# Performance work log

Hardware: AMD Instinct MI355X
Metric: run time of the kernel (lower is better)

## Reference

```python
import jax, jax.numpy as jnp
import numpy as np

VOCAB, EMBED, HIDDEN, POL = 32000, 300, 1024, 3
BS, SEQ = 64, 512


def setup_inputs() -> dict:
    key = jax.random.key(0)
    ks = jax.random.split(key, 17)
    stdv = 1.0 / np.sqrt(HIDDEN)
    u = lambda k, shape: jax.random.uniform(k, shape, jnp.float32, -stdv, stdv)
    return {
        "text": jax.random.randint(ks[0], (BS, SEQ), 0, VOCAB),
        "embed_table": jax.random.normal(ks[1], (VOCAB, EMBED), jnp.float32),
        "U_i": u(ks[2], (EMBED, HIDDEN)), "U_f": u(ks[3], (EMBED, HIDDEN)),
        "U_c": u(ks[4], (EMBED, HIDDEN)), "U_o": u(ks[5], (EMBED, HIDDEN)),
        "V_i": u(ks[6], (HIDDEN, HIDDEN)), "V_f": u(ks[7], (HIDDEN, HIDDEN)),
        "V_c": u(ks[8], (HIDDEN, HIDDEN)), "V_o": u(ks[9], (HIDDEN, HIDDEN)),
        "b_i": u(ks[10], (HIDDEN,)), "b_f": u(ks[11], (HIDDEN,)),
        "b_c": u(ks[12], (HIDDEN,)), "b_o": u(ks[13], (HIDDEN,)),
        "W_dense": u(ks[14], (HIDDEN, POL)),
        "b_dense": u(ks[15], (POL,)),
    }


def _lstm_final_h(x, U_i, U_f, U_c, U_o, V_i, V_f, V_c, V_o, b_i, b_f, b_c, b_o):
    # x: [B, S, E]. Precompute all input projections once (big fused GEMM),
    # leaving only the recurrent h @ V matmuls inside the scan.
    bs = x.shape[0]
    H = V_i.shape[0]
    U = jnp.concatenate([U_i, U_f, U_c, U_o], axis=1)          # [E, 4H]
    b = jnp.concatenate([b_i, b_f, b_c, b_o], axis=0)          # [4H]
    xU = jnp.einsum('bse,eh->sbh', x, U) + b                   # [S, B, 4H]
    V = jnp.concatenate([V_i, V_f, V_c, V_o], axis=1)          # [H, 4H]

    def step(carry, xu_t):
        h, c = carry
        gates = xu_t + h @ V                                   # [B, 4H]
        xi, xf, xg, xo = jnp.split(gates, 4, axis=-1)
        i = jax.nn.sigmoid(xi)
        f = jax.nn.sigmoid(xf)
        g = jnp.tanh(xg)
        o = jax.nn.sigmoid(xo)
        c = f * c + i * g
        h = o * jnp.tanh(c)
        return (h, c), None

    h0 = jnp.zeros((bs, H), x.dtype)
    c0 = jnp.zeros((bs, H), x.dtype)
    (h_n, c_n), _ = jax.lax.scan(step, (h0, c0), xU)
    return h_n


def reference(text, embed_table, U_i, U_f, U_c, U_o, V_i, V_f, V_c, V_o,
              b_i, b_f, b_c, b_o, W_dense, b_dense):
    x = embed_table[text]                                      # [B, S, E]
    h_n = _lstm_final_h(x, U_i, U_f, U_c, U_o, V_i, V_f, V_c, V_o,
                        b_i, b_f, b_c, b_o)                    # [B, H]
    return h_n @ W_dense + b_dense                             # [B, POL]
```

## Files before the change

kernel.cpp:

```cpp
#include <hip/hip_runtime.h>
#include <stdint.h>

#define SEQL 512
#define BATCH 64
#define EMB 300
#define EMBP 320
#define HID 1024
#define NWG 64
#define UNITS 16
#define NCH 42

typedef __attribute__((ext_vector_type(8))) short short8;
typedef __attribute__((ext_vector_type(4))) float f32x4;
typedef __attribute__((ext_vector_type(2))) unsigned int uint2v;

union Frag { short8 v; ushort u[8]; uint uu[4]; };
struct AF { uint2v lo, hi; };

__device__ __forceinline__ ushort f2bf(float f){
  union { float f; uint u; } c; c.f = f;
  return (ushort)((c.u + 0x7fffu + ((c.u >> 16) & 1u)) >> 16);
}

struct Params {
  const ushort* xbf;
  ushort* hbuf;
  float*  hfinal;
  int*    flags;
  ushort* wpack;
  const float* V[4];
  const float* U[4];
  const float* bia[4];
  const float* Wd;
  const float* bd;
  float* out;
};

__global__ void __launch_bounds__(256) prep(const int* __restrict__ text,
                                            const float* __restrict__ tab,
                                            ushort* __restrict__ xbf,
                                            ushort* __restrict__ hbuf,
                                            int* __restrict__ flags){
  const int tid = blockIdx.x * blockDim.x + threadIdx.x;
  const int nth = gridDim.x * blockDim.x;
  uint* hz = (uint*)hbuf;
  for (int i = tid; i < NWG*64*16/2; i += nth) hz[i] = 0u;
  if (tid < NWG) flags[tid] = 0;
  const int nch = SEQL*BATCH*(EMBP/8);
  for (int ch = tid; ch < nch; ch += nth){
    const int e8 = ch % (EMBP/8);
    const int sb = ch / (EMBP/8);
    const int b  = sb & (BATCH-1);
    const int s  = sb >> 6;
    const int tok = text[b*SEQL + s];
    union { ushort u[8]; uint4 v; } o;
    #pragma unroll
    for (int j = 0; j < 8; j++){
      const int e = e8*8 + j;
      o.u[j] = f2bf(e < EMB ? tab[(size_t)tok*EMB + e] : 0.f);
    }
    *(uint4*)&xbf[(size_t)sb*EMBP + e8*8] = o.v;
  }
}

__global__ void __launch_bounds__(256) packw(Params p){
  const int bid  = blockIdx.x;
  const int w    = bid / NCH;
  const int kc   = bid % NCH;
  const int tid  = threadIdx.x;
  const int nt   = tid >> 6;
  const int lane = tid & 63;
  const int l4   = (lane >> 4) & 3;
  const int colg = w*UNITS + (lane & 15);
  Frag fr;
  #pragma unroll
  for (int j = 0; j < 8; j++){
    const int koff = ((j >> 2) << 4) + l4*4 + (j & 3);
    float v = 0.f;
    if (kc < 32){
      v = p.V[nt][(size_t)(kc*32 + koff)*HID + colg];
    } else {
      const int krow = (kc-32)*32 + koff;
      if (krow < EMB) v = p.U[nt][(size_t)krow*HID + colg];
    }
    fr.u[j] = f2bf(v);
  }
  *(short8*)&p.wpack[(((size_t)(w*NCH + kc)*4 + nt)*64 + lane)*8] = fr.v;
}

#define WISSUE(c) { \
    const ushort* wp_ = wpk + (size_t)(wave + 4*(c))*2048 + lane*8; \
    asm volatile("global_load_dwordx4 %0, %4, off\n\t" \
                 "global_load_dwordx4 %1, %4, off offset:1024\n\t" \
                 "global_load_dwordx4 %2, %4, off offset:2048\n\t" \
                 "global_load_dwordx4 %3, %4, off offset:3072" \
                 : "=v"(wfr[(c)&3][0]), "=v"(wfr[(c)&3][1]), \
                   "=v"(wfr[(c)&3][2]), "=v"(wfr[(c)&3][3]) \
                 : "v"(wp_) : "memory"); }

#define VISSUE(c) { \
    const ushort* bp_ = hcur + (size_t)(wave + 4*(c))*2048 + qk; \
    _Pragma("unroll") \
    for (int m_ = 0; m_ < 4; m_++){ \
      const ushort* rp_ = bp_ + (m_*16 + mrow)*16; \
      asm volatile("global_load_dwordx2 %0, %2, off sc0 sc1\n\t" \
                   "global_load_dwordx2 %1, %2, off offset:2048 sc0 sc1" \
                   : "=v"(afr[(c)&3][m_].lo), "=v"(afr[(c)&3][m_].hi) \
                   : "v"(rp_) : "memory"); \
    } }

#define VWAIT(n) { asm volatile("s_waitcnt vmcnt(" #n ")" ::: "memory"); \
                   __builtin_amdgcn_sched_barrier(0); }

#define VMFMA(c) { \
    _Pragma("unroll") \
    for (int m_ = 0; m_ < 4; m_++){ \
      Frag a_; \
      a_.uu[0] = afr[(c)&3][m_].lo[0]; a_.uu[1] = afr[(c)&3][m_].lo[1]; \
      a_.uu[2] = afr[(c)&3][m_].hi[0]; a_.uu[3] = afr[(c)&3][m_].hi[1]; \
      _Pragma("unroll") \
      for (int nt_ = 0; nt_ < 4; nt_++) \
        acc[m_][nt_] = __builtin_amdgcn_mfma_f32_16x16x32_bf16(a_.v, wfr[(c)&3][nt_], acc[m_][nt_], 0, 0, 0); \
    } }

__global__ void __launch_bounds__(256, 1) lstm_scan(Params p){
  __shared__ float buffer[2][64][68];
  __shared__ float cst[UNITS][BATCH];
  __shared__ float bias_l[64];

  const int w    = blockIdx.x;
  const int tid  = threadIdx.x;
  const int wave = tid >> 6;
  const int lane = tid & 63;
  const int n0   = w * UNITS;
  const int mrow = lane & 15;
  const int qk   = ((lane >> 4) & 3) << 2;
  const int nU   = (wave < 2) ? 3 : 2;
  const ushort* __restrict__ wpk = p.wpack + (size_t)w*NCH*2048;

  const int pl   = lane & 15;
  const int* fp  = p.flags + 2*(wave + 4*(pl >> 1)) + (pl & 1);

  if (tid < 64) bias_l[tid] = p.bia[tid >> 4][n0 + (tid & 15)];
  for (int i = tid; i < UNITS*BATCH; i += 256) (&cst[0][0])[i] = 0.f;
  __syncthreads();

  for (int t = 0; t < SEQL; t++){
    const ushort* __restrict__ xt = p.xbf + (size_t)t * (BATCH*EMBP);

    f32x4 acc[4][4];
    #pragma unroll
    for (int m = 0; m < 4; m++)
      #pragma unroll
      for (int nt = 0; nt < 4; nt++)
        acc[m][nt] = (f32x4){0.f, 0.f, 0.f, 0.f};

    #pragma unroll
    for (int j3 = 0; j3 < 3; j3++){
      if (j3 < nU){
        const int kb  = (wave + 4*j3)*32;
        const int kcg = 32 + wave + 4*j3;
        Frag af[4];
        #pragma unroll
        for (int m = 0; m < 4; m++){
          const ushort* rp = xt + (size_t)(m*16 + mrow)*EMBP + kb + qk;
          uint2 lo = *(const uint2*)rp;
          uint2 hi = *(const uint2*)(rp + 16);
          af[m].uu[0] = lo.x; af[m].uu[1] = lo.y;
          af[m].uu[2] = hi.x; af[m].uu[3] = hi.y;
        }
        short8 wu[4];
        #pragma unroll
        for (int nt = 0; nt < 4; nt++)
          wu[nt] = *(const short8*)&wpk[(size_t)kcg*2048 + nt*512 + lane*8];
        #pragma unroll
        for (int m = 0; m < 4; m++)
          #pragma unroll
          for (int nt = 0; nt < 4; nt++)
            acc[m][nt] = __builtin_amdgcn_mfma_f32_16x16x32_bf16(af[m].v, wu[nt], acc[m][nt], 0, 0, 0);
      }
    }

    if (t > 0){
      for (;;){
        int v;
        asm volatile("global_load_dword %0, %1, off sc0 sc1\n\t"
                     "s_waitcnt vmcnt(0)"
                     : "=v"(v) : "v"(fp) : "memory");
        if (__all(v >= t)) break;
        __builtin_amdgcn_s_sleep(1);
      }
      __builtin_amdgcn_sched_barrier(0);

      const ushort* __restrict__ hcur = p.hbuf + (size_t)(t & 1) * (NWG*64*16);
      AF afr[4][4];
      short8 wfr[4][4];
      WISSUE(0) VISSUE(0) WISSUE(1) VISSUE(1)
      WISSUE(2) VISSUE(2) WISSUE(3) VISSUE(3)
      VWAIT(36) VMFMA(0) WISSUE(4) VISSUE(4)
      VWAIT(36) VMFMA(1) WISSUE(5) VISSUE(5)
      VWAIT(36) VMFMA(2) WISSUE(6) VISSUE(6)
      VWAIT(36) VMFMA(3) WISSUE(7) VISSUE(7)
      VWAIT(36) VMFMA(4)
      VWAIT(24) VMFMA(5)
      VWAIT(12) VMFMA(6)
      VWAIT(0)  VMFMA(7)
    }

    const int fq = (lane >> 4) << 2;
    if (wave >= 2){
      #pragma unroll
      for (int m = 0; m < 4; m++)
        #pragma unroll
        for (int nt = 0; nt < 4; nt++)
          *(f32x4*)&buffer[wave-2][nt*16 + mrow][m*16 + fq] = acc[m][nt];
    }
    __syncthreads();
    if (wave < 2){
      #pragma unroll
      for (int m = 0; m < 4; m++)
        #pragma unroll
        for (int nt = 0; nt < 4; nt++){
          f32x4 o = *(f32x4*)&buffer[wave][nt*16 + mrow][m*16 + fq];
          o += acc[m][nt];
          *(f32x4*)&buffer[wave][nt*16 + mrow][m*16 + fq] = o;
        }
    }
    __syncthreads();

    const int eb = tid & 63;
    const int uq = tid >> 6;
    ushort* __restrict__ hnxt = p.hbuf + (size_t)((t+1) & 1) * (NWG*64*16);
    ushort hout[4]; float hfv[4];
    #pragma unroll
    for (int rr = 0; rr < 4; rr++){
      const int u = uq*4 + rr;
      float g0 = buffer[0][ 0+u][eb] + buffer[1][ 0+u][eb] + bias_l[ 0+u];
      float g1 = buffer[0][16+u][eb] + buffer[1][16+u][eb] + bias_l[16+u];
      float g2 = buffer[0][32+u][eb] + buffer[1][32+u][eb] + bias_l[32+u];
      float g3 = buffer[0][48+u][eb] + buffer[1][48+u][eb] + bias_l[48+u];
      float ig = 1.f/(1.f + __expf(-g0));
      float fg = 1.f/(1.f + __expf(-g1));
      float gg = 2.f/(1.f + __expf(-2.f*g2)) - 1.f;
      float og = 1.f/(1.f + __expf(-g3));
      float cv = fg * cst[u][eb] + ig * gg;
      cst[u][eb] = cv;
      float hv = og * (2.f/(1.f + __expf(-2.f*cv)) - 1.f);
      hout[rr] = f2bf(hv);
      hfv[rr] = hv;
    }
    {
      union { ushort u[4]; uint2v v; } pk;
      pk.u[0]=hout[0]; pk.u[1]=hout[1]; pk.u[2]=hout[2]; pk.u[3]=hout[3];
      ushort* sa = &hnxt[(size_t)w*1024 + eb*16 + uq*4];
      asm volatile("global_store_dwordx2 %0, %1, off sc0 sc1"
                   :: "v"(sa), "v"(pk.v) : "memory");
      if (t == SEQL-1){
        f32x4 fv; fv[0]=hfv[0]; fv[1]=hfv[1]; fv[2]=hfv[2]; fv[3]=hfv[3];
        float* fa = &p.hfinal[(size_t)eb*HID + n0 + uq*4];
        asm volatile("global_store_dwordx4 %0, %1, off sc0 sc1"
                     :: "v"(fa), "v"(fv) : "memory");
      }
    }
    asm volatile("s_waitcnt vmcnt(0)" ::: "memory");
    __syncthreads();
    if (tid == 0){
      int tv = t + 1;
      asm volatile("global_store_dword %0, %1, off sc0 sc1"
                   :: "v"(p.flags + w), "v"(tv) : "memory");
    }
  }

  if (wave == 0){
    const int* ffp = p.flags + lane;
    for (;;){
      int v;
      asm volatile("global_load_dword %0, %1, off sc0 sc1\n\t"
                   "s_waitcnt vmcnt(0)"
                   : "=v"(v) : "v"(ffp) : "memory");
      if (__all(v >= SEQL)) break;
      __builtin_amdgcn_s_sleep(1);
    }
  }
  __syncthreads();

  float s0 = 0.f, s1 = 0.f, s2 = 0.f;
  const float* hf = p.hfinal + (size_t)w * HID;
  for (int k = tid; k < HID; k += 256){
    float hv;
    const float* ap = hf + k;
    asm volatile("global_load_dword %0, %1, off sc0 sc1\n\t"
                 "s_waitcnt vmcnt(0)"
                 : "=v"(hv) : "v"(ap) : "memory");
    s0 = fmaf(hv, p.Wd[k*3+0], s0);
    s1 = fmaf(hv, p.Wd[k*3+1], s1);
    s2 = fmaf(hv, p.Wd[k*3+2], s2);
  }
  float* red = &buffer[0][0][0];
  red[tid*3+0] = s0; red[tid*3+1] = s1; red[tid*3+2] = s2;
  __syncthreads();
  for (int off = 128; off > 0; off >>= 1){
    if (tid < off){
      red[tid*3+0] += red[(tid+off)*3+0];
      red[tid*3+1] += red[(tid+off)*3+1];
      red[tid*3+2] += red[(tid+off)*3+2];
    }
    __syncthreads();
  }
  if (tid < 3) p.out[w*3 + tid] = red[tid] + p.bd[tid];
}

extern "C" void kernel_launch(void* const* d_in, const int* in_sizes, int n_in,
                              void* d_out, int out_size, void* d_ws, size_t ws_size,
                              hipStream_t stream){
  const int*   text = (const int*)d_in[0];
  const float* tab  = (const float*)d_in[1];

  Params p;
  char* ws = (char*)d_ws;
  size_t off = 0;
  p.xbf    = (const ushort*)(ws + off); off += (size_t)SEQL*BATCH*EMBP*2;
  p.hbuf   = (ushort*)(ws + off);       off += (size_t)2*NWG*64*16*2;
  p.hfinal = (float*)(ws + off);        off += (size_t)BATCH*HID*4;
  p.flags  = (int*)(ws + off);          off += 256;
  p.wpack  = (ushort*)(ws + off);       off += (size_t)NWG*NCH*4*64*8*2;

  for (int g = 0; g < 4; g++){
    p.U[g]   = (const float*)d_in[2+g];
    p.V[g]   = (const float*)d_in[6+g];
    p.bia[g] = (const float*)d_in[10+g];
  }
  p.Wd  = (const float*)d_in[14];
  p.bd  = (const float*)d_in[15];
  p.out = (float*)d_out;

  prep<<<1024, 256, 0, stream>>>(text, tab, (ushort*)p.xbf, (ushort*)p.hbuf, p.flags);
  packw<<<NWG*NCH, 256, 0, stream>>>(p);
  lstm_scan<<<NWG, 256, 0, stream>>>(p);
}
```

Before: 4.074 ms.

## Pad per-workgroup flags to separate cache lines and harden inline-asm load constraints

Each workgroup's progress flag is now spaced 16 ints (64 bytes) apart instead of packed contiguously. This is meant to cut false sharing and contention on the cross-workgroup spin-wait flags polled every timestep. Inline-asm load outputs get early-clobber constraints, and a vmcnt(0) wait is added before the recurrent load pipeline; these fix possible register-aliasing and counter-accounting issues, at the cost of a small stall per step. The final dense reduction now issues its four hfinal loads together rather than one at a time.

```diff
diff --git a/kernel.cpp b/kernel.cpp
--- a/kernel.cpp
+++ b/kernel.cpp
@@ -9,6 +9,7 @@
 #define NWG 64
 #define UNITS 16
 #define NCH 42
+#define FSTR 16
 
 typedef __attribute__((ext_vector_type(8))) short short8;
 typedef __attribute__((ext_vector_type(4))) float f32x4;
@@ -45,7 +46,7 @@
   const int nth = gridDim.x * blockDim.x;
   uint* hz = (uint*)hbuf;
   for (int i = tid; i < NWG*64*16/2; i += nth) hz[i] = 0u;
-  if (tid < NWG) flags[tid] = 0;
+  if (tid < NWG*FSTR) flags[tid] = 0;
   const int nch = SEQL*BATCH*(EMBP/8);
   for (int ch = tid; ch < nch; ch += nth){
     const int e8 = ch % (EMBP/8);
@@ -94,8 +95,8 @@
                  "global_load_dwordx4 %1, %4, off offset:1024\n\t" \
                  "global_load_dwordx4 %2, %4, off offset:2048\n\t" \
                  "global_load_dwordx4 %3, %4, off offset:3072" \
-                 : "=v"(wfr[(c)&3][0]), "=v"(wfr[(c)&3][1]), \
-                   "=v"(wfr[(c)&3][2]), "=v"(wfr[(c)&3][3]) \
+                 : "=&v"(wfr[(c)&3][0]), "=&v"(wfr[(c)&3][1]), \
+                   "=&v"(wfr[(c)&3][2]), "=&v"(wfr[(c)&3][3]) \
                  : "v"(wp_) : "memory"); }
 
 #define VISSUE(c) { \
@@ -105,7 +106,7 @@
       const ushort* rp_ = bp_ + (m_*16 + mrow)*16; \
       asm volatile("global_load_dwordx2 %0, %2, off sc0 sc1\n\t" \
                    "global_load_dwordx2 %1, %2, off offset:2048 sc0 sc1" \
-                   : "=v"(afr[(c)&3][m_].lo), "=v"(afr[(c)&3][m_].hi) \
+                   : "=&v"(afr[(c)&3][m_].lo), "=&v"(afr[(c)&3][m_].hi) \
                    : "v"(rp_) : "memory"); \
     } }
 
@@ -139,7 +140,7 @@
   const ushort* __restrict__ wpk = p.wpack + (size_t)w*NCH*2048;
 
   const int pl   = lane & 15;
-  const int* fp  = p.flags + 2*(wave + 4*(pl >> 1)) + (pl & 1);
+  const int* fp  = p.flags + (2*(wave + 4*(pl >> 1)) + (pl & 1)) * FSTR;
 
   if (tid < 64) bias_l[tid] = p.bia[tid >> 4][n0 + (tid & 15)];
   for (int i = tid; i < UNITS*BATCH; i += 256) (&cst[0][0])[i] = 0.f;
@@ -186,7 +187,7 @@
         int v;
         asm volatile("global_load_dword %0, %1, off sc0 sc1\n\t"
                      "s_waitcnt vmcnt(0)"
-                     : "=v"(v) : "v"(fp) : "memory");
+                     : "=&v"(v) : "v"(fp) : "memory");
         if (__all(v >= t)) break;
         __builtin_amdgcn_s_sleep(1);
       }
@@ -195,6 +196,7 @@
       const ushort* __restrict__ hcur = p.hbuf + (size_t)(t & 1) * (NWG*64*16);
       AF afr[4][4];
       short8 wfr[4][4];
+      VWAIT(0)
       WISSUE(0) VISSUE(0) WISSUE(1) VISSUE(1)
       WISSUE(2) VISSUE(2) WISSUE(3) VISSUE(3)
       VWAIT(36) VMFMA(0) WISSUE(4) VISSUE(4)
@@ -267,17 +269,17 @@
     if (tid == 0){
       int tv = t + 1;
       asm volatile("global_store_dword %0, %1, off sc0 sc1"
-                   :: "v"(p.flags + w), "v"(tv) : "memory");
+                   :: "v"(p.flags + w*FSTR), "v"(tv) : "memory");
     }
   }
 
   if (wave == 0){
-    const int* ffp = p.flags + lane;
+    const int* ffp = p.flags + lane*FSTR;
     for (;;){
       int v;
       asm volatile("global_load_dword %0, %1, off sc0 sc1\n\t"
                    "s_waitcnt vmcnt(0)"
-                   : "=v"(v) : "v"(ffp) : "memory");
+                   : "=&v"(v) : "v"(ffp) : "memory");
       if (__all(v >= SEQL)) break;
       __builtin_amdgcn_s_sleep(1);
     }
@@ -285,16 +287,24 @@
   __syncthreads();
 
   float s0 = 0.f, s1 = 0.f, s2 = 0.f;
-  const float* hf = p.hfinal + (size_t)w * HID;
-  for (int k = tid; k < HID; k += 256){
-    float hv;
-    const float* ap = hf + k;
-    asm volatile("global_load_dword %0, %1, off sc0 sc1\n\t"
+  {
+    const float* ap = p.hfinal + (size_t)w * HID + tid;
+    float h0, h1, h2, h3;
+    asm volatile("global_load_dword %0, %4, off sc0 sc1\n\t"
+                 "global_load_dword %1, %4, off offset:1024 sc0 sc1\n\t"
+                 "global_load_dword %2, %4, off offset:2048 sc0 sc1\n\t"
+                 "global_load_dword %3, %4, off offset:3072 sc0 sc1\n\t"
                  "s_waitcnt vmcnt(0)"
-                 : "=v"(hv) : "v"(ap) : "memory");
-    s0 = fmaf(hv, p.Wd[k*3+0], s0);
-    s1 = fmaf(hv, p.Wd[k*3+1], s1);
-    s2 = fmaf(hv, p.Wd[k*3+2], s2);
+                 : "=&v"(h0), "=&v"(h1), "=&v"(h2), "=&v"(h3)
+                 : "v"(ap) : "memory");
+    const float hvv[4] = {h0, h1, h2, h3};
+    #pragma unroll
+    for (int j = 0; j < 4; j++){
+      const int k = tid + 256*j;
+      s0 = fmaf(hvv[j], p.Wd[k*3+0], s0);
+      s1 = fmaf(hvv[j], p.Wd[k*3+1], s1);
+      s2 = fmaf(hvv[j], p.Wd[k*3+2], s2);
+    }
   }
   float* red = &buffer[0][0][0];
   red[tid*3+0] = s0; red[tid*3+1] = s1; red[tid*3+2] = s2;
@@ -322,7 +332,7 @@
   p.xbf    = (const ushort*)(ws + off); off += (size_t)SEQL*BATCH*EMBP*2;
   p.hbuf   = (ushort*)(ws + off);       off += (size_t)2*NWG*64*16*2;
   p.hfinal = (float*)(ws + off);        off += (size_t)BATCH*HID*4;
-  p.flags  = (int*)(ws + off);          off += 256;
+  p.flags  = (int*)(ws + off);          off += (size_t)NWG*FSTR*4;
   p.wpack  = (ushort*)(ws + off);       off += (size_t)NWG*NCH*4*64*8*2;
 
   for (int g = 0; g < 4; g++){
```

After: 4.167 ms. +2.3%, slower.
